# Kernel optimization log

Measured on AMD Instinct MI355X. Metric: run time of the kernel, lower is better.

Reference implementation:

```python
import jax, jax.numpy as jnp
import numpy as np

# n-gram trie hyperparameters (match torch module invariants exactly)
V = 8192          # vocabulary size
N = 3             # n-gram order (trigram)
SHIFT = 0         # no sos/eos shift
C2, C3 = 32, 8    # children per unigram node / per bigram node
U = V + SHIFT + 1
B2 = U * C2                  # bigram node count
B3 = B2 * C3                 # trigram node count
X = U + B2 + 1               # pointers length (level 1..N-1 nodes + dummy)
G = B3 - 1
K = X + G - U                # ids length == B2 + B3
L = 2 * X + G                # logs length
S_MAX = max(C2, C3)          # static max branching factor (torch computes it dynamically)
BATCH = 128


def _build_trie():
    rng = np.random.RandomState(0)
    u = np.arange(U, dtype=np.int32)
    i = np.arange(B2, dtype=np.int32)
    # pointers[node] = first_child_index(node) - node; dummy last entry closes counts
    ptr_uni = (U + u.astype(np.int64) * C2 - u).astype(np.int32)
    ptr_bi = (B2 + i.astype(np.int64) * (C3 - 1)).astype(np.int32)
    pointers = np.concatenate([ptr_uni, ptr_bi, np.array([B3], dtype=np.int32)])
    # child token ids: distinct per parent (strides 251, 977 coprime-ish, C*stride < V)
    ids_bi = ((u[:, None].astype(np.int64) * 17 + np.arange(C2)[None, :] * 251) % V).reshape(-1).astype(np.int32)
    ids_tri = ((i[:, None].astype(np.int64) * 13 + np.arange(C3)[None, :] * 977) % V).reshape(-1).astype(np.int32)
    ids = np.concatenate([ids_bi, ids_tri])
    n_nodes = U + B2 + B3    # == X + G
    logs = np.concatenate([
        -rng.uniform(1.0, 10.0, n_nodes),   # conditional log-probs per node
        -rng.uniform(0.1, 2.0, X),          # backoff weights for nodes 0..X-1
    ]).astype(np.float32)
    assert ids.size == K and logs.size == L
    return jnp.asarray(pointers), jnp.asarray(ids), jnp.asarray(logs)


def setup_inputs() -> dict:
    key = jax.random.key(0)
    pointers, ids, logs = _build_trie()
    hist = jax.random.randint(key, (N - 1, BATCH), 0, V, dtype=jnp.int32)
    return {"hist": hist, "idx": N - 1, "pointers": pointers, "ids": ids, "logs": logs}


def _forward(hist, idx, pointers, ids, logs):
    B = hist.shape[1]
    M = B * V
    h = hist[:idx][-(N - 1):]                                 # (N-1, B), idx >= N-1
    vr = jnp.arange(V, dtype=hist.dtype)
    cur = jnp.broadcast_to(vr[None, None, :], (1, B, V))
    h = jnp.concatenate(
        [jnp.broadcast_to(h[:, :, None], (N - 1, B, V)), cur], 0
    ).reshape(N, M)                                           # (N, M) token grid

    srange = jnp.arange(S_MAX, dtype=jnp.int32)
    out = jnp.zeros(M, jnp.float32)
    running = jnp.ones(M, bool)
    children = tokens = h[0]
    for Nn in range(N - 1):
        n = N - Nn
        offsets = pointers[children]
        num_children = pointers[children + 1] - offsets + 1
        first_children = children + offsets
        step_mask = running
        for t in range(1, n):
            tokens = h[Nn + t]
            all_children = first_children[:, None] + srange[None, :]  # (M, S_MAX)
            matches = (
                (ids[jnp.clip(all_children, None, K + U - 1) - U] == tokens[:, None])
                & (srange[None, :] < num_children[:, None])
                & step_mask[:, None]
            )
            next_step = matches.any(1)
            if t == n - 1:
                logs_t = jnp.where(matches, logs[all_children], 0.0).sum(1)
                finite = jnp.isfinite(logs_t)
                out = jnp.where(finite, out + logs_t, out)
                next_step = next_step & finite
                running = running & ~next_step
                new_backoff = step_mask & ~next_step
                out = jnp.where(new_backoff, out + logs[X + G + children], out)
            else:
                children = jnp.where(matches, all_children, 0).sum(1)
                offsets = pointers[children]
                num_children = pointers[children + 1] - offsets + 1
                first_children = children + offsets
            step_mask = next_step
        children = tokens = h[Nn + 1]
    out = jnp.where(running, out + logs[tokens], out)
    return out.reshape(B, V)


def reference(hist, idx, pointers, ids, logs):
    return _forward(hist, idx, pointers, ids, logs)
```

## Files before the change

### kernel.cpp

```cpp
#include <hip/hip_runtime.h>

#define TV   8192
#define TU   8193
#define TXP  270370
#define TG   2097407
#define TKU  2367776
#define CHUNKS 8
#define VCHUNK (TV / CHUNKS)
#define SENT 0x7F800000u

__global__ __launch_bounds__(256) void lookup_lm_kernel(
    const int* __restrict__ hist, const int* __restrict__ idxp,
    const int* __restrict__ pointers, const int* __restrict__ ids,
    const float* __restrict__ logs, float* __restrict__ out, int Bsz)
{
    __shared__ unsigned s_over[VCHUNK];
    __shared__ int   s_ptr[33];
    __shared__ float s_base;
    __shared__ float s_bo1;
    __shared__ int   s_ctx;

    const int tid   = threadIdx.x;
    const int b     = blockIdx.y;
    const int vbase = blockIdx.x * VCHUNK;

    float4 lg4 = *reinterpret_cast<const float4*>(logs + vbase + tid * 4);
    int h0  = hist[b];
    int h1  = hist[Bsz + b];
    int idx = idxp[0];
    if (idx != 2) {
        h0 = hist[(idx - 2) * Bsz + b];
        h1 = hist[(idx - 1) * Bsz + b];
    }

    *reinterpret_cast<uint4*>(&s_over[tid * 4]) = make_uint4(SENT, SENT, SENT, SENT);
    if (tid == 0) s_ctx = -1;

    const int p_h0  = pointers[h0];
    const int p_h0n = pointers[h0 + 1];
    const int p_h1  = pointers[h1];
    const int p_h1n = pointers[h1 + 1];

    const int fc0  = h0 + p_h0;
    const int nch0 = p_h0n - p_h0 + 1;
    const int fcb  = h1 + p_h1;
    const int nchb = p_h1n - p_h1 + 1;

    __syncthreads();

    int big_id = -1; float big_log = 0.f;
    if (tid < 32) {
        if (tid < nch0) {
            int node = fc0 + tid;
            int cid  = ids[min(node, TKU) - TU];
            if (cid == h1) s_ctx = node;
        }
    } else if (tid < 64) {
        int s = tid - 32;
        if (s < nchb) {
            int node = fcb + s;
            big_id  = ids[min(node, TKU) - TU];
            big_log = logs[node];
        }
    } else if (tid < 97) {
        s_ptr[tid - 64] = pointers[fc0 + (tid - 64)];
    } else if (tid == 97) {
        s_bo1 = logs[TXP + TG + h1];
    }
    __syncthreads();

    const int ctx = s_ctx;
    int tri_id = -1; float tri_log = 0.f;
    if (ctx >= 0) {
        if (tid < 8) {
            int ci   = ctx - fc0;
            int offc = s_ptr[ci];
            int nchc = s_ptr[ci + 1] - offc + 1;
            if (tid < nchc) {
                int node = ctx + offc + tid;
                tri_id  = ids[min(node, TKU) - TU];
                tri_log = logs[node];
            }
        } else if (tid == 8) {
            s_base = logs[TXP + TG + ctx];
        }
    } else if (tid == 8) {
        s_base = 0.f;
    }
    __syncthreads();

    const float base = s_base;

    if (big_id >= vbase && big_id < vbase + VCHUNK) {
        s_over[big_id - vbase] = __float_as_uint(base + big_log);
    }
    __syncthreads();
    if (tri_id >= vbase && tri_id < vbase + VCHUNK) {
        s_over[tri_id - vbase] = __float_as_uint(tri_log);
    }
    __syncthreads();

    const float fb = base + s_bo1;
    uint4 ov = *reinterpret_cast<const uint4*>(&s_over[tid * 4]);
    float4 res;
    res.x = (ov.x == SENT) ? fb + lg4.x : __uint_as_float(ov.x);
    res.y = (ov.y == SENT) ? fb + lg4.y : __uint_as_float(ov.y);
    res.z = (ov.z == SENT) ? fb + lg4.z : __uint_as_float(ov.z);
    res.w = (ov.w == SENT) ? fb + lg4.w : __uint_as_float(ov.w);
    *reinterpret_cast<float4*>(out + (size_t)b * TV + vbase + tid * 4) = res;
}

extern "C" void kernel_launch(void* const* d_in, const int* in_sizes, int n_in,
                              void* d_out, int out_size, void* d_ws, size_t ws_size,
                              hipStream_t stream) {
    const int*   hist     = (const int*)d_in[0];
    const int*   idxp     = (const int*)d_in[1];
    const int*   pointers = (const int*)d_in[2];
    const int*   ids      = (const int*)d_in[3];
    const float* logs     = (const float*)d_in[4];
    float* out = (float*)d_out;

    const int B = in_sizes[0] / 2;
    dim3 grid(CHUNKS, B);
    lookup_lm_kernel<<<grid, 256, 0, stream>>>(hist, idxp, pointers, ids, logs, out, B);
}
```

Baseline: 10.06 us.

## Speculatively prefetch trigram children and context backoffs to shorten dependent load chain

The kernel now guesses where every candidate bigram context's trigram children live, assuming the regular trie layout, and loads their ids and logs for all 32 contexts in parallel with the first-level lookups. It also loads the backoff weights of all 32 candidate contexts up front, so no extra global load is needed once the matching context is known. The fixed 8-children-per-context layout is only a speculation: when the actual offset differs, the code falls back to loading the children directly, so the result stays correct. This removes two serialized global-memory round trips and one barrier, at the cost of many extra speculative loads per block.

Measured after the change: 18.34 us. +82.3%, slower.

```diff
diff --git a/kernel.cpp b/kernel.cpp
--- a/kernel.cpp
+++ b/kernel.cpp
@@ -2,9 +2,10 @@
 
 #define TV   8192
 #define TU   8193
-#define TXP  270370
-#define TG   2097407
+#define TB2  262176
+#define TXG  2367777
 #define TKU  2367776
+#define TL   2638147
 #define CHUNKS 8
 #define VCHUNK (TV / CHUNKS)
 #define SENT 0x7F800000u
@@ -16,7 +17,7 @@
 {
     __shared__ unsigned s_over[VCHUNK];
     __shared__ int   s_ptr[33];
-    __shared__ float s_base;
+    __shared__ float s_cbk[32];
     __shared__ float s_bo1;
     __shared__ int   s_ctx;
 
@@ -32,71 +33,75 @@
         h0 = hist[(idx - 2) * Bsz + b];
         h1 = hist[(idx - 1) * Bsz + b];
     }
-
     *reinterpret_cast<uint4*>(&s_over[tid * 4]) = make_uint4(SENT, SENT, SENT, SENT);
     if (tid == 0) s_ctx = -1;
 
-    const int p_h0  = pointers[h0];
-    const int p_h0n = pointers[h0 + 1];
-    const int p_h1  = pointers[h1];
-    const int p_h1n = pointers[h1 + 1];
+    const int p0  = pointers[h0];
+    const int p0n = pointers[h0 + 1];
+    const int p1  = pointers[h1];
+    const int p1n = pointers[h1 + 1];
+    const int fc0  = h0 + p0;
+    const int nch0 = p0n - p0 + 1;
+    const int fcb  = h1 + p1;
+    const int nchb = p1n - p1 + 1;
 
-    const int fc0  = h0 + p_h0;
-    const int nch0 = p_h0n - p_h0 + 1;
-    const int fcb  = h1 + p_h1;
-    const int nchb = p_h1n - p_h1 + 1;
+    const int ci = tid >> 3, t = tid & 7;
+    const int pred = TU + TB2 + 8 * (fc0 - TU + ci) + t;
+    const int pid  = ids[min(pred, TKU) - TU];
+    const float plog = logs[min(max(pred, 0), TL - 1)];
+
+    int cid = -1, big_id = -1; float big_log = 0.f, cbk = 0.f; int ptrv = 0;
+    if (tid < 32) {
+        if (tid < nch0) cid = ids[min(fc0 + tid, TKU) - TU];
+        if (tid < nchb) {
+            int node = fcb + tid;
+            big_id  = ids[min(node, TKU) - TU];
+            big_log = logs[node];
+        }
+        cbk = logs[TXG + fc0 + tid];
+    }
+    if (tid < 33) ptrv = pointers[fc0 + tid];
+    float bo1v = (tid == 33) ? logs[TXG + h1] : 0.f;
 
     __syncthreads();
 
-    int big_id = -1; float big_log = 0.f;
-    if (tid < 32) {
-        if (tid < nch0) {
-            int node = fc0 + tid;
-            int cid  = ids[min(node, TKU) - TU];
-            if (cid == h1) s_ctx = node;
-        }
-    } else if (tid < 64) {
-        int s = tid - 32;
-        if (s < nchb) {
-            int node = fcb + s;
-            big_id  = ids[min(node, TKU) - TU];
-            big_log = logs[node];
-        }
-    } else if (tid < 97) {
-        s_ptr[tid - 64] = pointers[fc0 + (tid - 64)];
-    } else if (tid == 97) {
-        s_bo1 = logs[TXP + TG + h1];
-    }
+    if (tid < 32) { s_cbk[tid] = cbk; if (cid == h1) s_ctx = fc0 + tid; }
+    if (tid < 33) s_ptr[tid] = ptrv;
+    if (tid == 33) s_bo1 = bo1v;
     __syncthreads();
 
-    const int ctx = s_ctx;
-    int tri_id = -1; float tri_log = 0.f;
-    if (ctx >= 0) {
-        if (tid < 8) {
-            int ci   = ctx - fc0;
-            int offc = s_ptr[ci];
-            int nchc = s_ptr[ci + 1] - offc + 1;
-            if (tid < nchc) {
-                int node = ctx + offc + tid;
-                tri_id  = ids[min(node, TKU) - TU];
-                tri_log = logs[node];
-            }
-        } else if (tid == 8) {
-            s_base = logs[TXP + TG + ctx];
-        }
-    } else if (tid == 8) {
-        s_base = 0.f;
-    }
+    const int   ctx  = s_ctx;
+    const float base = (ctx >= 0) ? s_cbk[ctx - fc0] : 0.f;
+
+    if ((unsigned)(big_id - vbase) < VCHUNK)
+        s_over[big_id - vbase] = __float_as_uint(base + big_log);
     __syncthreads();
 
-    const float base = s_base;
-
-    if (big_id >= vbase && big_id < vbase + VCHUNK) {
-        s_over[big_id - vbase] = __float_as_uint(base + big_log);
-    }
-    __syncthreads();
-    if (tri_id >= vbase && tri_id < vbase + VCHUNK) {
-        s_over[tri_id - vbase] = __float_as_uint(tri_log);
+    if (ctx >= 0 && ci == ctx - fc0) {
+        const int offc   = s_ptr[ci];
+        const int nchc   = s_ptr[ci + 1] - offc + 1;
+        const int afirst = ctx + offc;
+        const int pfirst = pred - t;
+        const int lim    = min(nchc, 32);
+        if (afirst == pfirst) {
+            if (t < lim && (unsigned)(pid - vbase) < VCHUNK)
+                s_over[pid - vbase] = __float_as_uint(plog);
+            for (int t2 = 8 + t; t2 < lim; t2 += 8) {
+                int node = afirst + t2;
+                int id2 = ids[min(node, TKU) - TU];
+                float l2 = logs[node];
+                if ((unsigned)(id2 - vbase) < VCHUNK)
+                    s_over[id2 - vbase] = __float_as_uint(l2);
+            }
+        } else {
+            for (int t2 = t; t2 < lim; t2 += 8) {
+                int node = afirst + t2;
+                int id2 = ids[min(node, TKU) - TU];
+                float l2 = logs[node];
+                if ((unsigned)(id2 - vbase) < VCHUNK)
+                    s_over[id2 - vbase] = __float_as_uint(l2);
+            }
+        }
     }
     __syncthreads();
 
```
